# Performance work log

Hardware: AMD Instinct MI355X
Metric: run time of the kernel (lower is better)

## Reference

```python
import jax, jax.numpy as jnp
import numpy as np

N_VERTICES = 100000
N_EDGES = 25000
NNZ = 3200000
IN_CH = 256
OUT_CH = 128


def setup_inputs() -> dict:
    key = jax.random.key(0)
    k1, k2, k3, k4, k5 = jax.random.split(key, 5)
    X = jax.random.normal(k1, (N_VERTICES, IN_CH), dtype=jnp.float32)
    W = jax.random.normal(k2, (OUT_CH, IN_CH), dtype=jnp.float32) * 0.05
    b = jax.random.normal(k3, (OUT_CH,), dtype=jnp.float32) * 0.05
    v_idx = jax.random.randint(k4, (NNZ,), 0, N_VERTICES, dtype=jnp.int32)
    e_idx = jax.random.randint(k5, (NNZ,), 0, N_EDGES, dtype=jnp.int32)
    return {"X": X, "W": W, "b": b, "v_idx": v_idx, "e_idx": e_idx}


def reference(X, W, b, v_idx, e_idx):
    # theta(X).relu().detach()
    H = jnp.maximum(jnp.einsum('nc,oc->no', X, W) + b, 0.0)  # [N, out]
    H = jax.lax.stop_gradient(H)

    ones = jnp.ones((NNZ,), dtype=H.dtype)
    # v2e with mean aggregation: gather vertex feats to incidence, segment-mean per hyperedge
    msg_ve = H[v_idx]                                           # [nnz, out]
    e_sum = jax.ops.segment_sum(msg_ve, e_idx, num_segments=N_EDGES)
    e_deg = jax.ops.segment_sum(ones, e_idx, num_segments=N_EDGES)
    e_feat = e_sum / jnp.maximum(e_deg, 1.0)[:, None]           # [E, out]

    # e2v with mean aggregation: gather edge feats back, segment-mean per vertex
    msg_ev = e_feat[e_idx]                                      # [nnz, out]
    v_sum = jax.ops.segment_sum(msg_ev, v_idx, num_segments=N_VERTICES)
    v_deg = jax.ops.segment_sum(ones, v_idx, num_segments=N_VERTICES)
    out = v_sum / jnp.maximum(v_deg, 1.0)[:, None]              # [N, out]

    # not is_last: ReLU (dropout rate 0 -> identity in eval)
    return jnp.maximum(out, 0.0)
```

## Files before the change

### kernel.cpp

```cpp
#include <hip/hip_runtime.h>
#include <hip/hip_bf16.h>

constexpr int NV  = 100000;
constexpr int NE  = 25000;
constexpr int NNZ = 3200000;
constexpr int IC  = 256;
constexpr int OC  = 128;

constexpr int LSH_E = 5;
constexpr int NBUCK_E = (NE + 31) / 32;
constexpr int LSH_V = 7;
constexpr int NBUCK_V = (NV + 127) / 128;
constexpr int CAP = 4608;
constexpr int NBUCK_MAX = 782;

constexpr int NPB = (NNZ + 4095) / 4096;
constexpr int NGB = (NV + 63) / 64;

constexpr float HSCALE = 6.0f;
constexpr float HQ     = 255.0f / HSCALE;

typedef __attribute__((ext_vector_type(8))) short short8;
typedef __attribute__((ext_vector_type(4))) float f32x4;

__device__ __forceinline__ unsigned pack_bf2(float a, float b) {
  unsigned ua = __float_as_uint(a), ub = __float_as_uint(b);
  unsigned ra = (ua + 0x7fffu + ((ua >> 16) & 1u)) >> 16;
  unsigned rb = (ub + 0x7fffu + ((ub >> 16) & 1u)) >> 16;
  return ra | (rb << 16);
}

__global__ __launch_bounds__(512) void k_prep(const float* __restrict__ W,
                                              unsigned short* __restrict__ Wbf,
                                              int* __restrict__ gcur_e,
                                              int* __restrict__ gcur_v) {
  const int b = blockIdx.x, t = threadIdx.x;
  if (b < 16) {
    int idx = (b * 512 + t) * 4;
    float4 f = *reinterpret_cast<const float4*>(&W[idx]);
    uint2 p;
    p.x = pack_bf2(f.x, f.y);
    p.y = pack_bf2(f.z, f.w);
    *reinterpret_cast<uint2*>(&Wbf[idx]) = p;
  } else {
    for (int i = t; i < NBUCK_E; i += 512) gcur_e[i] = 0;
    for (int i = t; i < NBUCK_V; i += 512) gcur_v[i] = 0;
  }
}


template <int NBUCK, int LSH>
__device__ __forceinline__ void part_phase(const int (&key)[8], const int (&oth)[8],
                                           int n, unsigned* __restrict__ out,
                                           int* __restrict__ gcur,
                                           int* hist, int* hist2, int* lstart, int* gbase,
                                           unsigned* spay, unsigned short* sbkt,
                                           int* wtot, int t) {
  for (int b = t; b < NBUCK; b += 512) { hist[b] = 0; hist2[b] = 0; }
  __syncthreads();
  const int lane = t & 63, wv = t >> 6;
  int* myh = (wv < 4) ? hist : hist2;
  int myb[8], myr[8];
#pragma unroll
  for (int q = 0; q < 8; ++q) {
    int lin = 4 * (t + 512 * (q >> 2)) + (q & 3);
    if (lin < n) { myb[q] = key[q] >> LSH; myr[q] = atomicAdd(&myh[myb[q]], 1); }
    else myb[q] = -1;
  }
  __syncthreads();
  constexpr int K = (NBUCK + 511) / 512;
  int b0 = t * K, lsum = 0;
#pragma unroll
  for (int j = 0; j < K; ++j) { int b = b0 + j; if (b < NBUCK) lsum += hist[b] + hist2[b]; }
  int incl = lsum;
#pragma unroll
  for (int o = 1; o < 64; o <<= 1) {
    int up = __shfl_up(incl, o, 64);
    if (lane >= o) incl += up;
  }
  if (lane == 63) wtot[wv] = incl;
  __syncthreads();
  int wofs = 0;
  for (int i = 0; i < wv; ++i) wofs += wtot[i];
  int run = wofs + incl - lsum;
#pragma unroll
  for (int j = 0; j < K; ++j) {
    int b = b0 + j;
    if (b < NBUCK) { lstart[b] = run; run += hist[b] + hist2[b]; }
  }
  __syncthreads();
  const int grp2 = (wv >= 4);
#pragma unroll
  for (int q = 0; q < 8; ++q) {
    if (myb[q] >= 0) {
      int pos = lstart[myb[q]] + myr[q] + (grp2 ? hist[myb[q]] : 0);
      spay[pos] = ((unsigned)oth[q] << LSH) | (unsigned)(key[q] & ((1 << LSH) - 1));
      sbkt[pos] = (unsigned short)myb[q];
    }
  }
  for (int b = t; b < NBUCK; b += 512) {
    int c = hist[b] + hist2[b];
    gbase[b] = c ? atomicAdd(&gcur[b], c) : 0;
  }
  __syncthreads();
  for (int i = t; i < n; i += 512) {
    int b = sbkt[i];
    int ofs = gbase[b] + (i - lstart[b]);
    if (ofs < CAP) out[(size_t)b * CAP + ofs] = spay[i];
  }
}

__global__ __launch_bounds__(512) void k_part_gemm(const int* __restrict__ v_idx,
                                                   const int* __restrict__ e_idx,
                                                   unsigned* __restrict__ out_e,
                                                   int* __restrict__ gcur_e,
                                                   unsigned* __restrict__ out_v,
                                                   int* __restrict__ gcur_v,
                                                   const float* __restrict__ X,
                                                   const unsigned short* __restrict__ Wbf,
                                                   const float* __restrict__ bias,
                                                   unsigned char* __restrict__ H) {
  __shared__ __align__(16) union {
    struct {
      int hist[NBUCK_MAX], hist2[NBUCK_MAX], lstart[NBUCK_MAX], gbase[NBUCK_MAX];
      unsigned spay[4096];
      unsigned short sbkt[4096];
      int wtot[8];
    } p;
    struct {
      unsigned short Al[64 * 72];
      unsigned short Wl[128 * 72];
    } g;
  } sh;
  const int bid = blockIdx.x;
  const int t = threadIdx.x;

  if (bid % 3 == 0) {
    const int pid = bid / 3;
    const int base = pid * 4096;
    const int n = min(4096, NNZ - base);
    int kv[8], ke[8];
#pragma unroll
    for (int q = 0; q < 2; ++q) {
      int lin = 4 * (t + 512 * q);
      if (lin < n) {
        *reinterpret_cast<int4*>(&kv[q * 4]) = *reinterpret_cast<const int4*>(&v_idx[base + lin]);
        *reinterpret_cast<int4*>(&ke[q * 4]) = *reinterpret_cast<const int4*>(&e_idx[base + lin]);
      } else {
#pragma unroll
        for (int u = 0; u < 4; ++u) { kv[q * 4 + u] = 0; ke[q * 4 + u] = 0; }
      }
    }
    part_phase<NBUCK_E, LSH_E>(ke, kv, n, out_e, gcur_e,
                               sh.p.hist, sh.p.hist2, sh.p.lstart, sh.p.gbase,
                               sh.p.spay, sh.p.sbkt, sh.p.wtot, t);
    __syncthreads();
    part_phase<NBUCK_V, LSH_V>(kv, ke, n, out_v, gcur_v,
                               sh.p.hist, sh.p.hist2, sh.p.lstart, sh.p.gbase,
                               sh.p.spay, sh.p.sbkt, sh.p.wtot, t);
  } else {
    const int gid = bid - bid / 3 - 1;
    const int row0 = gid * 64;
    const int w = t >> 6, l = t & 63;
    const int wr = w >> 1, wc = w & 1;
    const int fr = l & 15, fq = l >> 4;

    f32x4 acc[4];
#pragma unroll
    for (int n = 0; n < 4; ++n) acc[n] = (f32x4){0.f, 0.f, 0.f, 0.f};

    for (int kc = 0; kc < IC; kc += 64) {
      {
        int r = t >> 3, k0 = (t & 7) * 8;
        uint4 p;
        int grow = row0 + r;
        if (grow < NV) {
          const float4 f0 = *reinterpret_cast<const float4*>(&X[(size_t)grow * IC + kc + k0]);
          const float4 f1 = *reinterpret_cast<const float4*>(&X[(size_t)grow * IC + kc + k0 + 4]);
          p.x = pack_bf2(f0.x, f0.y); p.y = pack_bf2(f0.z, f0.w);
          p.z = pack_bf2(f1.x, f1.y); p.w = pack_bf2(f1.z, f1.w);
        } else {
          p = (uint4){0, 0, 0, 0};
        }
        *reinterpret_cast<uint4*>(&sh.g.Al[(size_t)r * 72 + k0]) = p;
      }
#pragma unroll
      for (int i = 0; i < 2; ++i) {
        int c = t + 512 * i;
        int r = c >> 3, k0 = (c & 7) * 8;
        uint4 q = *reinterpret_cast<const uint4*>(&Wbf[(size_t)r * IC + kc + k0]);
        *reinterpret_cast<uint4*>(&sh.g.Wl[(size_t)r * 72 + k0]) = q;
      }
      __syncthreads();
#pragma unroll
      for (int ks = 0; ks < 2; ++ks) {
        short8 av, bv[4];
        av = *reinterpret_cast<const short8*>(&sh.g.Al[(size_t)(wr * 16 + fr) * 72 + ks * 32 + fq * 8]);
#pragma unroll
        for (int n = 0; n < 4; ++n)
          bv[n] = *reinterpret_cast<const short8*>(&sh.g.Wl[(size_t)(wc * 64 + n * 16 + fr) * 72 + ks * 32 + fq * 8]);
#pragma unroll
        for (int n = 0; n < 4; ++n)
          acc[n] = __builtin_amdgcn_mfma_f32_16x16x32_bf16(av, bv[n], acc[n], 0, 0, 0);
      }
      __syncthreads();
    }

    float bb[4];
#pragma unroll
    for (int n = 0; n < 4; ++n) bb[n] = bias[wc * 64 + n * 16 + fr];
#pragma unroll
    for (int j = 0; j < 4; ++j) {
      int grow = row0 + wr * 16 + fq * 4 + j;
      if (grow < NV) {
        unsigned b[4];
#pragma unroll
        for (int n = 0; n < 4; ++n) {
          float v = fmaxf(acc[n][j] + bb[n], 0.f);
          b[n] = (unsigned)fminf(v * HQ + 0.5f, 255.0f);
        }
        unsigned u = b[0] | (b[1] << 8) | (b[2] << 16) | (b[3] << 24);
        *reinterpret_cast<unsigned*>(&H[(size_t)grow * OC + wc * 64 + fr * 4]) = u;
      }
    }
  }
}

__global__ __launch_bounds__(512) void k_consE_sortV(const unsigned* __restrict__ part_e,
                                                     const int* __restrict__ gcur_e,
                                                     const unsigned char* __restrict__ Hsrc,
                                                     unsigned char* __restrict__ e_feat,
                                                     unsigned* __restrict__ part_v,
                                                     const int* __restrict__ gcur_v,
                                                     int* __restrict__ begin_v,
                                                     int* __restrict__ cnt_v) {
  __shared__ unsigned staged[CAP];
  __shared__ int hist[128], start[128];
  __shared__ int wtot[8];
  const int bid = blockIdx.x;
  const int t = threadIdx.x;
  const int lane = t & 63, wv = t >> 6;

  if (bid < NBUCK_E) {
    constexpr int W = 32;
    const int b = bid;
    const int n = min(gcur_e[b], CAP);
    const unsigned* __restrict__ sp = part_e + (size_t)b * CAP;

    if (t < W) hist[t] = 0;
    __syncthreads();
    unsigned rp[9]; int rr[9];
#pragma unroll
    for (int q = 0; q < 9; ++q) {
      int i = t + 512 * q;
      if (i < n) { rp[q] = sp[i]; rr[q] = atomicAdd(&hist[rp[q] & (W - 1)], 1); }
      else rr[q] = -1;
    }
    __syncthreads();
    {
      int lsum = (t < W) ? hist[t] : 0;
      int incl = lsum;
#pragma unroll
      for (int o = 1; o < 64; o <<= 1) {
        int up = __shfl_up(incl, o, 64);
        if (lane >= o) incl += up;
      }
      if (lane == 63) wtot[wv] = incl;
      __syncthreads();
      int wofs = 0;
      for (int i = 0; i < wv; ++i) wofs += wtot[i];
      if (t < W) start[t] = wofs + incl - lsum;
    }
    __syncthreads();
#pragma unroll
    for (int q = 0; q < 9; ++q)
      if (rr[q] >= 0) staged[start[rp[q] & (W - 1)] + rr[q]] = rp[q] >> LSH_E;
    __syncthreads();

    const int quad = t >> 5, s = t & 31;
    const unsigned* __restrict__ srcw = reinterpret_cast<const unsigned*>(Hsrc);
    constexpr unsigned M = 0x00FF00FFu;
    for (int l = quad; l < W; l += 16) {
      const int st = start[l], m = hist[l];
      unsigned accL = 0, accH = 0;
      int j = 0;
      for (; j + 4 <= m; j += 4) {
        unsigned r0 = staged[st + j],     r1 = staged[st + j + 1];
        unsigned r2 = staged[st + j + 2], r3 = staged[st + j + 3];
        unsigned u0 = srcw[(size_t)r0 * 32 + s];
        unsigned u1 = srcw[(size_t)r1 * 32 + s];
        unsigned u2 = srcw[(size_t)r2 * 32 + s];
        unsigned u3 = srcw[(size_t)r3 * 32 + s];
        accL += ((u0 & M) + (u1 & M)) + ((u2 & M) + (u3 & M));
        accH += (((u0 >> 8) & M) + ((u1 >> 8) & M)) + (((u2 >> 8) & M) + ((u3 >> 8) & M));
      }
      for (; j < m; ++j) {
        unsigned u = srcw[(size_t)staged[st + j] * 32 + s];
        accL += (u & M);
        accH += ((u >> 8) & M);
      }
      const int seg = b * W + l;
      if (seg < NE) {
        const int ch = (s & 15) + ((s >> 4) * 64);
        float inv = HSCALE / (float)max(m, 1);
        unsigned char* d = e_feat + (size_t)seg * OC + ch;
        d[ 0] = (unsigned char)fminf((float)(accL & 0xFFFFu) * inv + 0.5f, 255.0f);
        d[16] = (unsigned char)fminf((float)(accH & 0xFFFFu) * inv + 0.5f, 255.0f);
        d[32] = (unsigned char)fminf((float)(accL >> 16)     * inv + 0.5f, 255.0f);
        d[48] = (unsigned char)fminf((float)(accH >> 16)     * inv + 0.5f, 255.0f);
      }
    }
  } else {
    constexpr int W = 128;
    const int b = bid - NBUCK_E;
    const int n = min(gcur_v[b], CAP);
    unsigned* __restrict__ sp = part_v + (size_t)b * CAP;

    if (t < W) hist[t] = 0;
    __syncthreads();
    unsigned rp[9]; int rr[9];
#pragma unroll
    for (int q = 0; q < 9; ++q) {
      int i = t + 512 * q;
      if (i < n) { rp[q] = sp[i]; rr[q] = atomicAdd(&hist[rp[q] & (W - 1)], 1); }
      else rr[q] = -1;
    }
    __syncthreads();
    {
      int lsum = (t < W) ? hist[t] : 0;
      int incl = lsum;
#pragma unroll
      for (int o = 1; o < 64; o <<= 1) {
        int up = __shfl_up(incl, o, 64);
        if (lane >= o) incl += up;
      }
      if (lane == 63) wtot[wv] = incl;
      __syncthreads();
      int wofs = 0;
      for (int i = 0; i < wv; ++i) wofs += wtot[i];
      if (t < W) start[t] = wofs + incl - lsum;
    }
    __syncthreads();
#pragma unroll
    for (int q = 0; q < 9; ++q)
      if (rr[q] >= 0) staged[start[rp[q] & (W - 1)] + rr[q]] = rp[q] >> LSH_V;
    __syncthreads();
    for (int i = t; i < n; i += 512) sp[i] = staged[i];
    if (t < W) {
      int seg = b * W + t;
      if (seg < NV) { begin_v[seg] = b * CAP + start[t]; cnt_v[seg] = hist[t]; }
    }
  }
}

__global__ __launch_bounds__(256) void k_gather_v(const unsigned char* __restrict__ src,
                                                  const int* __restrict__ begin,
                                                  const int* __restrict__ cnt,
                                                  const unsigned* __restrict__ csr,
                                                  float* __restrict__ dst) {
  const int seg = blockIdx.x * 8 + (threadIdx.x >> 5);
  if (seg >= NV) return;
  const int s = threadIdx.x & 31;
  const int st = begin[seg];
  const int m = cnt[seg];
  const unsigned* __restrict__ srcw = reinterpret_cast<const unsigned*>(src);
  unsigned accL = 0, accH = 0;
  constexpr unsigned M = 0x00FF00FFu;

  int j = 0;
  for (; j + 4 <= m; j += 4) {
    unsigned r0 = csr[st + j], r1 = csr[st + j + 1];
    unsigned r2 = csr[st + j + 2], r3 = csr[st + j + 3];
    unsigned u0 = srcw[(size_t)r0 * 32 + s];
    unsigned u1 = srcw[(size_t)r1 * 32 + s];
    unsigned u2 = srcw[(size_t)r2 * 32 + s];
    unsigned u3 = srcw[(size_t)r3 * 32 + s];
    accL += ((u0 & M) + (u1 & M)) + ((u2 & M) + (u3 & M));
    accH += (((u0 >> 8) & M) + ((u1 >> 8) & M)) + (((u2 >> 8) & M) + ((u3 >> 8) & M));
  }
  for (; j < m; ++j) {
    unsigned u = srcw[(size_t)csr[st + j] * 32 + s];
    accL += (u & M);
    accH += ((u >> 8) & M);
  }

  float inv = 1.0f / (255.0f * (float)max(m, 1));
  float4 o;
  o.x = (float)(accL & 0xFFFFu) * inv;
  o.y = (float)(accH & 0xFFFFu) * inv;
  o.z = (float)(accL >> 16)     * inv;
  o.w = (float)(accH >> 16)     * inv;
  *reinterpret_cast<float4*>(&dst[(size_t)seg * OC + 4 * s]) = o;
}

extern "C" void kernel_launch(void* const* d_in, const int* in_sizes, int n_in,
                              void* d_out, int out_size, void* d_ws, size_t ws_size,
                              hipStream_t stream) {
  const float* X    = (const float*)d_in[0];
  const float* W    = (const float*)d_in[1];
  const float* bias = (const float*)d_in[2];
  const int* v_idx  = (const int*)d_in[3];
  const int* e_idx  = (const int*)d_in[4];
  float* out = (float*)d_out;

  char* ws = (char*)d_ws;
  size_t off = 0;
  auto alloc = [&](size_t bytes) -> void* {
    void* p = ws + off;
    off = (off + bytes + 255) & ~(size_t)255;
    return p;
  };
  unsigned char* H       = (unsigned char*)alloc((size_t)NV * OC);
  unsigned char* e_feat  = (unsigned char*)alloc((size_t)NE * OC);
  unsigned* part_e       = (unsigned*)alloc((size_t)NBUCK_E * CAP * 4);
  unsigned* part_v       = (unsigned*)alloc((size_t)NBUCK_V * CAP * 4);
  unsigned short* Wbf    = (unsigned short*)alloc((size_t)OC * IC * 2);
  int* begin_v     = (int*)alloc((size_t)NV * 4);
  int* cnt_v       = (int*)alloc((size_t)NV * 4);
  int* gcur_e      = (int*)alloc((size_t)NBUCK_E * 4);
  int* gcur_v      = (int*)alloc((size_t)NBUCK_V * 4);

  k_prep<<<17, 512, 0, stream>>>(W, Wbf, gcur_e, gcur_v);

  k_part_gemm<<<NPB + NGB, 512, 0, stream>>>(v_idx, e_idx, part_e, gcur_e, part_v, gcur_v,
                                             X, Wbf, bias, H);

  k_consE_sortV<<<NBUCK_E + NBUCK_V, 512, 0, stream>>>(part_e, gcur_e, H, e_feat,
                                                       part_v, gcur_v, begin_v, cnt_v);

  k_gather_v<<<(NV + 7) / 8, 256, 0, stream>>>(e_feat, begin_v, cnt_v, part_v, out);
}
```

Baseline: 159.8 us.

## Split edge and vertex gathers by channel half to overlap stages

The edge-consumption stage now computes only the first 64 channels of e_feat and writes a sorted edge CSR. A new kernel computes the remaining edge channels at the same time as the first half of the vertex gather, which only needs the first-half e_feat. A final kernel gathers the second half of the vertex output. Each segment now uses two lane groups that each take alternate rows, and the partial sums are combined with a shuffle. The aim is to shorten the serial dependency chain and raise memory-level parallelism, at the cost of an extra launch, extra CSR writes and reading each index list twice.

```diff
diff --git a/kernel.cpp b/kernel.cpp
--- a/kernel.cpp
+++ b/kernel.cpp
@@ -16,6 +16,8 @@
 
 constexpr int NPB = (NNZ + 4095) / 4096;
 constexpr int NGB = (NV + 63) / 64;
+constexpr int NEB = (NE + 15) / 16;
+constexpr int NVB = (NV + 15) / 16;
 
 constexpr float HSCALE = 6.0f;
 constexpr float HQ     = 255.0f / HSCALE;
@@ -47,7 +49,6 @@
     for (int i = t; i < NBUCK_V; i += 512) gcur_v[i] = 0;
   }
 }
-
 
 template <int NBUCK, int LSH>
 __device__ __forceinline__ void part_phase(const int (&key)[8], const int (&oth)[8],
@@ -226,14 +227,44 @@
   }
 }
 
-__global__ __launch_bounds__(512) void k_consE_sortV(const unsigned* __restrict__ part_e,
-                                                     const int* __restrict__ gcur_e,
-                                                     const unsigned char* __restrict__ Hsrc,
-                                                     unsigned char* __restrict__ e_feat,
-                                                     unsigned* __restrict__ part_v,
-                                                     const int* __restrict__ gcur_v,
-                                                     int* __restrict__ begin_v,
-                                                     int* __restrict__ cnt_v) {
+__device__ __forceinline__ void gather_half(const unsigned* __restrict__ srcw,
+                                            const unsigned* __restrict__ csr,
+                                            int st, int m, int cu, int g2,
+                                            unsigned& accL, unsigned& accH) {
+  constexpr unsigned M = 0x00FF00FFu;
+  int j = 0;
+  for (; j + 8 <= m; j += 8) {
+    unsigned r0 = csr[st + j + g2];
+    unsigned r1 = csr[st + j + 2 + g2];
+    unsigned r2 = csr[st + j + 4 + g2];
+    unsigned r3 = csr[st + j + 6 + g2];
+    unsigned u0 = srcw[(size_t)r0 * 32 + cu];
+    unsigned u1 = srcw[(size_t)r1 * 32 + cu];
+    unsigned u2 = srcw[(size_t)r2 * 32 + cu];
+    unsigned u3 = srcw[(size_t)r3 * 32 + cu];
+    accL += ((u0 & M) + (u1 & M)) + ((u2 & M) + (u3 & M));
+    accH += (((u0 >> 8) & M) + ((u1 >> 8) & M)) + (((u2 >> 8) & M) + ((u3 >> 8) & M));
+  }
+  for (; j < m; j += 2) {
+    int idx = j + g2;
+    if (idx < m) {
+      unsigned u = srcw[(size_t)csr[st + idx] * 32 + cu];
+      accL += (u & M);
+      accH += ((u >> 8) & M);
+    }
+  }
+}
+
+__global__ __launch_bounds__(512) void k_stage2(unsigned* __restrict__ part_e,
+                                                const int* __restrict__ gcur_e,
+                                                const unsigned char* __restrict__ Hsrc,
+                                                unsigned char* __restrict__ e_feat,
+                                                int* __restrict__ begin_e,
+                                                int* __restrict__ cnt_e,
+                                                unsigned* __restrict__ part_v,
+                                                const int* __restrict__ gcur_v,
+                                                int* __restrict__ begin_v,
+                                                int* __restrict__ cnt_v) {
   __shared__ unsigned staged[CAP];
   __shared__ int hist[128], start[128];
   __shared__ int wtot[8];
@@ -245,7 +276,7 @@
     constexpr int W = 32;
     const int b = bid;
     const int n = min(gcur_e[b], CAP);
-    const unsigned* __restrict__ sp = part_e + (size_t)b * CAP;
+    unsigned* __restrict__ sp = part_e + (size_t)b * CAP;
 
     if (t < W) hist[t] = 0;
     __syncthreads();
@@ -276,34 +307,46 @@
     for (int q = 0; q < 9; ++q)
       if (rr[q] >= 0) staged[start[rp[q] & (W - 1)] + rr[q]] = rp[q] >> LSH_E;
     __syncthreads();
+    for (int i = t; i < n; i += 512) sp[i] = staged[i];
+    if (t < W) {
+      int seg = b * W + t;
+      if (seg < NE) { begin_e[seg] = b * CAP + start[t]; cnt_e[seg] = hist[t]; }
+    }
 
     const int quad = t >> 5, s = t & 31;
+    const int cu = s & 15, g2 = s >> 4;
     const unsigned* __restrict__ srcw = reinterpret_cast<const unsigned*>(Hsrc);
     constexpr unsigned M = 0x00FF00FFu;
     for (int l = quad; l < W; l += 16) {
       const int st = start[l], m = hist[l];
       unsigned accL = 0, accH = 0;
       int j = 0;
-      for (; j + 4 <= m; j += 4) {
-        unsigned r0 = staged[st + j],     r1 = staged[st + j + 1];
-        unsigned r2 = staged[st + j + 2], r3 = staged[st + j + 3];
-        unsigned u0 = srcw[(size_t)r0 * 32 + s];
-        unsigned u1 = srcw[(size_t)r1 * 32 + s];
-        unsigned u2 = srcw[(size_t)r2 * 32 + s];
-        unsigned u3 = srcw[(size_t)r3 * 32 + s];
+      for (; j + 8 <= m; j += 8) {
+        unsigned r0 = staged[st + j + g2];
+        unsigned r1 = staged[st + j + 2 + g2];
+        unsigned r2 = staged[st + j + 4 + g2];
+        unsigned r3 = staged[st + j + 6 + g2];
+        unsigned u0 = srcw[(size_t)r0 * 32 + cu];
+        unsigned u1 = srcw[(size_t)r1 * 32 + cu];
+        unsigned u2 = srcw[(size_t)r2 * 32 + cu];
+        unsigned u3 = srcw[(size_t)r3 * 32 + cu];
         accL += ((u0 & M) + (u1 & M)) + ((u2 & M) + (u3 & M));
         accH += (((u0 >> 8) & M) + ((u1 >> 8) & M)) + (((u2 >> 8) & M) + ((u3 >> 8) & M));
       }
-      for (; j < m; ++j) {
-        unsigned u = srcw[(size_t)staged[st + j] * 32 + s];
-        accL += (u & M);
-        accH += ((u >> 8) & M);
-      }
+      for (; j < m; j += 2) {
+        int idx = j + g2;
+        if (idx < m) {
+          unsigned u = srcw[(size_t)staged[st + idx] * 32 + cu];
+          accL += (u & M);
+          accH += ((u >> 8) & M);
+        }
+      }
+      accL += __shfl_xor(accL, 16, 32);
+      accH += __shfl_xor(accH, 16, 32);
       const int seg = b * W + l;
-      if (seg < NE) {
-        const int ch = (s & 15) + ((s >> 4) * 64);
+      if (seg < NE && g2 == 0) {
         float inv = HSCALE / (float)max(m, 1);
-        unsigned char* d = e_feat + (size_t)seg * OC + ch;
+        unsigned char* d = e_feat + (size_t)seg * OC + cu;
         d[ 0] = (unsigned char)fminf((float)(accL & 0xFFFFu) * inv + 0.5f, 255.0f);
         d[16] = (unsigned char)fminf((float)(accH & 0xFFFFu) * inv + 0.5f, 255.0f);
         d[32] = (unsigned char)fminf((float)(accL >> 16)     * inv + 0.5f, 255.0f);
@@ -353,44 +396,80 @@
   }
 }
 
-__global__ __launch_bounds__(256) void k_gather_v(const unsigned char* __restrict__ src,
-                                                  const int* __restrict__ begin,
-                                                  const int* __restrict__ cnt,
-                                                  const unsigned* __restrict__ csr,
-                                                  float* __restrict__ dst) {
-  const int seg = blockIdx.x * 8 + (threadIdx.x >> 5);
+__global__ __launch_bounds__(512) void k_stage3(const unsigned char* __restrict__ Hsrc,
+                                                const unsigned* __restrict__ csr_e,
+                                                const int* __restrict__ begin_e,
+                                                const int* __restrict__ cnt_e,
+                                                unsigned char* __restrict__ e_feat,
+                                                const unsigned* __restrict__ csr_v,
+                                                const int* __restrict__ begin_v,
+                                                const int* __restrict__ cnt_v,
+                                                float* __restrict__ out) {
+  const int bid = blockIdx.x;
+  const int t = threadIdx.x;
+  const int quad = t >> 5, s = t & 31;
+  const int cu = s & 15, g2 = s >> 4;
+
+  if (bid % 5 == 0) {
+    const int seg = (bid / 5) * 16 + quad;
+    if (seg >= NE) return;
+    const int st = begin_e[seg], m = cnt_e[seg];
+    unsigned accL = 0, accH = 0;
+    gather_half(reinterpret_cast<const unsigned*>(Hsrc), csr_e, st, m, 16 + cu, g2, accL, accH);
+    accL += __shfl_xor(accL, 16, 32);
+    accH += __shfl_xor(accH, 16, 32);
+    if (g2 == 0) {
+      float inv = HSCALE / (float)max(m, 1);
+      unsigned char* d = e_feat + (size_t)seg * OC + 64 + cu;
+      d[ 0] = (unsigned char)fminf((float)(accL & 0xFFFFu) * inv + 0.5f, 255.0f);
+      d[16] = (unsigned char)fminf((float)(accH & 0xFFFFu) * inv + 0.5f, 255.0f);
+      d[32] = (unsigned char)fminf((float)(accL >> 16)     * inv + 0.5f, 255.0f);
+      d[48] = (unsigned char)fminf((float)(accH >> 16)     * inv + 0.5f, 255.0f);
+    }
+  } else {
+    const int seg = (bid - bid / 5 - 1) * 16 + quad;
+    if (seg >= NV) return;
+    const int st = begin_v[seg], m = cnt_v[seg];
+    unsigned accL = 0, accH = 0;
+    gather_half(reinterpret_cast<const unsigned*>(e_feat), csr_v, st, m, cu, g2, accL, accH);
+    accL += __shfl_xor(accL, 16, 32);
+    accH += __shfl_xor(accH, 16, 32);
+    if (g2 == 0) {
+      float inv = 1.0f / (255.0f * (float)max(m, 1));
+      float4 o;
+      o.x = (float)(accL & 0xFFFFu) * inv;
+      o.y = (float)(accH & 0xFFFFu) * inv;
+      o.z = (float)(accL >> 16)     * inv;
+      o.w = (float)(accH >> 16)     * inv;
+      *reinterpret_cast<float4*>(&out[(size_t)seg * OC + 4 * cu]) = o;
+    }
+  }
+}
+
+__global__ __launch_bounds__(512) void k_stage4(const unsigned char* __restrict__ e_feat,
+                                                const unsigned* __restrict__ csr_v,
+                                                const int* __restrict__ begin_v,
+                                                const int* __restrict__ cnt_v,
+                                                float* __restrict__ out) {
+  const int t = threadIdx.x;
+  const int quad = t >> 5, s = t & 31;
+  const int cu = s & 15, g2 = s >> 4;
+  const int seg = blockIdx.x * 16 + quad;
   if (seg >= NV) return;
-  const int s = threadIdx.x & 31;
-  const int st = begin[seg];
-  const int m = cnt[seg];
-  const unsigned* __restrict__ srcw = reinterpret_cast<const unsigned*>(src);
+  const int st = begin_v[seg], m = cnt_v[seg];
   unsigned accL = 0, accH = 0;
-  constexpr unsigned M = 0x00FF00FFu;
-
-  int j = 0;
-  for (; j + 4 <= m; j += 4) {
-    unsigned r0 = csr[st + j], r1 = csr[st + j + 1];
-    unsigned r2 = csr[st + j + 2], r3 = csr[st + j + 3];
-    unsigned u0 = srcw[(size_t)r0 * 32 + s];
-    unsigned u1 = srcw[(size_t)r1 * 32 + s];
-    unsigned u2 = srcw[(size_t)r2 * 32 + s];
-    unsigned u3 = srcw[(size_t)r3 * 32 + s];
-    accL += ((u0 & M) + (u1 & M)) + ((u2 & M) + (u3 & M));
-    accH += (((u0 >> 8) & M) + ((u1 >> 8) & M)) + (((u2 >> 8) & M) + ((u3 >> 8) & M));
-  }
-  for (; j < m; ++j) {
-    unsigned u = srcw[(size_t)csr[st + j] * 32 + s];
-    accL += (u & M);
-    accH += ((u >> 8) & M);
-  }
-
-  float inv = 1.0f / (255.0f * (float)max(m, 1));
-  float4 o;
-  o.x = (float)(accL & 0xFFFFu) * inv;
-  o.y = (float)(accH & 0xFFFFu) * inv;
-  o.z = (float)(accL >> 16)     * inv;
-  o.w = (float)(accH >> 16)     * inv;
-  *reinterpret_cast<float4*>(&dst[(size_t)seg * OC + 4 * s]) = o;
+  gather_half(reinterpret_cast<const unsigned*>(e_feat), csr_v, st, m, 16 + cu, g2, accL, accH);
+  accL += __shfl_xor(accL, 16, 32);
+  accH += __shfl_xor(accH, 16, 32);
+  if (g2 == 0) {
+    float inv = 1.0f / (255.0f * (float)max(m, 1));
+    float4 o;
+    o.x = (float)(accL & 0xFFFFu) * inv;
+    o.y = (float)(accH & 0xFFFFu) * inv;
+    o.z = (float)(accL >> 16)     * inv;
+    o.w = (float)(accH >> 16)     * inv;
+    *reinterpret_cast<float4*>(&out[(size_t)seg * OC + 64 + 4 * cu]) = o;
+  }
 }
 
 extern "C" void kernel_launch(void* const* d_in, const int* in_sizes, int n_in,
@@ -415,6 +494,8 @@
   unsigned* part_e       = (unsigned*)alloc((size_t)NBUCK_E * CAP * 4);
   unsigned* part_v       = (unsigned*)alloc((size_t)NBUCK_V * CAP * 4);
   unsigned short* Wbf    = (unsigned short*)alloc((size_t)OC * IC * 2);
+  int* begin_e     = (int*)alloc((size_t)NE * 4);
+  int* cnt_e       = (int*)alloc((size_t)NE * 4);
   int* begin_v     = (int*)alloc((size_t)NV * 4);
   int* cnt_v       = (int*)alloc((size_t)NV * 4);
   int* gcur_e      = (int*)alloc((size_t)NBUCK_E * 4);
@@ -425,8 +506,11 @@
   k_part_gemm<<<NPB + NGB, 512, 0, stream>>>(v_idx, e_idx, part_e, gcur_e, part_v, gcur_v,
                                              X, Wbf, bias, H);
 
-  k_consE_sortV<<<NBUCK_E + NBUCK_V, 512, 0, stream>>>(part_e, gcur_e, H, e_feat,
-                                                       part_v, gcur_v, begin_v, cnt_v);
-
-  k_gather_v<<<(NV + 7) / 8, 256, 0, stream>>>(e_feat, begin_v, cnt_v, part_v, out);
-}
+  k_stage2<<<NBUCK_E + NBUCK_V, 512, 0, stream>>>(part_e, gcur_e, H, e_feat, begin_e, cnt_e,
+                                                  part_v, gcur_v, begin_v, cnt_v);
+
+  k_stage3<<<NEB + NVB, 512, 0, stream>>>(H, part_e, begin_e, cnt_e, e_feat,
+                                          part_v, begin_v, cnt_v, out);
+
+  k_stage4<<<NVB, 512, 0, stream>>>(e_feat, part_v, begin_v, cnt_v, out);
+}
```

New measurement: 253.0 us. +58.3%, slower.
